# Kernel tuning notes

Measured on AMD Instinct MI355X. Metric: run time of the kernel, lower is better.

Reference implementation:

```python
import jax, jax.numpy as jnp
import numpy as np

# Module hyperparameters (from init_kwargs)
NUM_NEURONS = 16384
BATCH = 2048  # processed sequentially, sharing neuron state
V_TH0 = 1.0
V_RESET = 0.0
TAU = 20.0
DT = 1.0
ETA = 0.1
NOISE_STD = 0.1
MIN_TH = 0.5
MAX_TH = 2.0
USE_ADAPTIVE = True
STOCHASTIC = True


def setup_inputs() -> dict:
    key = jax.random.key(0)
    k1, k2 = jax.random.split(key)
    input_current = jax.random.normal(k1, (BATCH, NUM_NEURONS), dtype=jnp.float32)
    # stochastic membrane noise, pre-sampled for determinism
    noise = NOISE_STD * jax.random.normal(k2, (BATCH, NUM_NEURONS), dtype=jnp.float32)
    if not STOCHASTIC:
        noise = jnp.zeros_like(noise)
    return {"input_current": input_current, "noise": noise}


def reference(input_current, noise):
    # Faithful to the torch wrapper: each batch row is fed through the SAME
    # LIFNeuronGroup sequentially, carrying membrane potential V and the
    # adaptive threshold V_th across rows -> lax.scan over the batch axis.
    n = input_current.shape[1]
    V0 = jnp.full((n,), V_RESET, dtype=jnp.float32)
    Vth0 = jnp.full((n,), V_TH0, dtype=jnp.float32)

    def step(carry, inp):
        V, Vth = carry
        I, nz = inp
        # leaky integration + noise injection (fused elementwise)
        V = V + (DT / TAU) * (I - V) + nz
        spikes = V >= Vth
        V = jnp.where(spikes, V_RESET, V)
        if USE_ADAPTIVE:
            Vth = jnp.clip(Vth + ETA * spikes.astype(jnp.float32), MIN_TH, MAX_TH)
        return (V, Vth), spikes.astype(jnp.float32)

    (_, _), out_spikes = jax.lax.scan(step, (V0, Vth0), (input_current, noise))
    return out_spikes  # [batch, num_neurons] binary float32
```

## Files before the change

### kernel.cpp

```cpp
#include <hip/hip_runtime.h>


constexpr int N  = 16384;
constexpr int T  = 2048;
constexpr int U  = 16;
constexpr int NC = T / U;
constexpr int S  = 12;
constexpr int NP = 7;

__global__
__attribute__((amdgpu_flat_work_group_size(512, 512)))
void TorchLIFNeuronGroup_85152021610615_kernel(const float* __restrict__ I,
                                               const float* __restrict__ Z,
                                               float* __restrict__ O) {
    #pragma clang fp contract(off)
    __shared__ float ring[S][2][U][64];
    __shared__ int   flags[NC];
    __shared__ int   cons;

    if (threadIdx.x < NC) flags[threadIdx.x] = 0;
    if (threadIdx.x == 0) cons = -1;
    __syncthreads();

    const int wave = threadIdx.x >> 6;
    const int lane = threadIdx.x & 63;
    const int nb   = blockIdx.x * 64 + lane;

    if (wave >= 1) {
        const int p = wave - 1;
        const float* gI = I + nb;
        const float* gZ = Z + nb;

        for (int k = p; k < NC; k += NP) {
            while (__hip_atomic_load(&cons, __ATOMIC_RELAXED,
                                     __HIP_MEMORY_SCOPE_WORKGROUP) < k - S)
                __builtin_amdgcn_s_sleep(1);
            __asm__ volatile("" ::: "memory");

            const int    slot = k % S;
            const size_t t0   = (size_t)k * U;
            float vi[U], vz[U];
            #pragma unroll
            for (int u = 0; u < U; ++u) {
                vi[u] = gI[(t0 + u) * N];
                vz[u] = gZ[(t0 + u) * N];
            }
            #pragma unroll
            for (int u = 0; u < U; ++u) {
                ring[slot][0][u][lane] = vi[u];
                ring[slot][1][u][lane] = vz[u];
            }
            __asm__ volatile("s_waitcnt lgkmcnt(0)" ::: "memory");
            if (lane == 0)
                __hip_atomic_store(&flags[k], 1, __ATOMIC_RELAXED,
                                   __HIP_MEMORY_SCOPE_WORKGROUP);
        }

    } else {
        float* op = O + nb;
        float V   = 0.0f;
        float Vth = 1.0f;
        float ai[U], az[U], bi[U], bz[U];

        while (__hip_atomic_load(&flags[0], __ATOMIC_ACQUIRE,
                                 __HIP_MEMORY_SCOPE_WORKGROUP) == 0)
            __builtin_amdgcn_s_sleep(1);
        #pragma unroll
        for (int u = 0; u < U; ++u) { ai[u] = ring[0][0][u][lane]; az[u] = ring[0][1][u][lane]; }

        for (int k = 0; k < NC; k += 2) {
            while (__hip_atomic_load(&flags[k + 1], __ATOMIC_ACQUIRE,
                                     __HIP_MEMORY_SCOPE_WORKGROUP) == 0)
                __builtin_amdgcn_s_sleep(1);
            {
                const int slot = (k + 1) % S;
                #pragma unroll
                for (int u = 0; u < U; ++u) { bi[u] = ring[slot][0][u][lane]; bz[u] = ring[slot][1][u][lane]; }
            }
            #pragma unroll
            for (int u = 0; u < U; ++u) {
                #pragma clang fp contract(off)
                float d  = ai[u] - V;
                float v1 = V + 0.05f * d;
                float v2 = v1 + az[u];
                bool  s  = (v2 >= Vth);
                V = s ? 0.0f : v2;
                float nth = fminf(fmaxf(Vth + 0.1f, 0.5f), 2.0f);
                Vth = s ? nth : Vth;
                op[(size_t)(k * U + u) * N] = s ? 1.0f : 0.0f;
            }
            __asm__ volatile("s_waitcnt lgkmcnt(0)" ::: "memory");
            if (lane == 0)
                __hip_atomic_store(&cons, k, __ATOMIC_RELAXED,
                                   __HIP_MEMORY_SCOPE_WORKGROUP);

            if (k + 2 < NC) {
                while (__hip_atomic_load(&flags[k + 2], __ATOMIC_ACQUIRE,
                                         __HIP_MEMORY_SCOPE_WORKGROUP) == 0)
                    __builtin_amdgcn_s_sleep(1);
                const int slot = (k + 2) % S;
                #pragma unroll
                for (int u = 0; u < U; ++u) { ai[u] = ring[slot][0][u][lane]; az[u] = ring[slot][1][u][lane]; }
            }
            #pragma unroll
            for (int u = 0; u < U; ++u) {
                #pragma clang fp contract(off)
                float d  = bi[u] - V;
                float v1 = V + 0.05f * d;
                float v2 = v1 + bz[u];
                bool  s  = (v2 >= Vth);
                V = s ? 0.0f : v2;
                float nth = fminf(fmaxf(Vth + 0.1f, 0.5f), 2.0f);
                Vth = s ? nth : Vth;
                op[(size_t)((k + 1) * U + u) * N] = s ? 1.0f : 0.0f;
            }
            __asm__ volatile("s_waitcnt lgkmcnt(0)" ::: "memory");
            if (lane == 0)
                __hip_atomic_store(&cons, k + 1, __ATOMIC_RELAXED,
                                   __HIP_MEMORY_SCOPE_WORKGROUP);
        }
    }
}

extern "C" void kernel_launch(void* const* d_in, const int* in_sizes, int n_in,
                              void* d_out, int out_size, void* d_ws, size_t ws_size,
                              hipStream_t stream) {
    const float* input_current = (const float*)d_in[0];
    const float* noise         = (const float*)d_in[1];
    float* out                 = (float*)d_out;

    TorchLIFNeuronGroup_85152021610615_kernel<<<N / 64, 512, 0, stream>>>(
        input_current, noise, out);
}
```

Before: 326.4 us.

## Vectorize producer loads to float4, prefetch before ring wait, deepen ring

Producer waves now load input and noise as float4 tiles, with 16 lanes covering a 64-neuron row and four rows per wave. This replaces per-lane scalar loads, and the global loads are issued before the wait for a free ring slot so their latency overlaps the wait. The ring grows from 12 to 16 slots with power-of-two indexing. The consumer drops its mid-pair 'cons' publish and uses relaxed flag loads with compiler barriers. These changes are meant to cut load instruction count and stalls, in exchange for more LDS use and coarser slot-release granularity. Because loads now happen before the slot is confirmed free, correctness depends on the larger ring and the remaining per-pair cons update.

After: 343.9 us. 1.05x slower.

```diff
diff --git a/kernel.cpp b/kernel.cpp
--- a/kernel.cpp
+++ b/kernel.cpp
@@ -5,7 +5,7 @@
 constexpr int T  = 2048;
 constexpr int U  = 16;
 constexpr int NC = T / U;
-constexpr int S  = 12;
+constexpr int S  = 16;
 constexpr int NP = 7;
 
 __global__
@@ -14,7 +14,8 @@
                                                const float* __restrict__ Z,
                                                float* __restrict__ O) {
     #pragma clang fp contract(off)
-    __shared__ float ring[S][2][U][64];
+    __shared__ float ringI[S][U][64];
+    __shared__ float ringZ[S][U][64];
     __shared__ int   flags[NC];
     __shared__ int   cons;
 
@@ -24,31 +25,32 @@
 
     const int wave = threadIdx.x >> 6;
     const int lane = threadIdx.x & 63;
-    const int nb   = blockIdx.x * 64 + lane;
 
-    if (wave >= 1) {
+    if (wave != 0) {
         const int p = wave - 1;
-        const float* gI = I + nb;
-        const float* gZ = Z + nb;
+        const int r = lane >> 4;
+        const int c = lane & 15;
+        const float* bI = I + (size_t)blockIdx.x * 64 + 4 * c;
+        const float* bZ = Z + (size_t)blockIdx.x * 64 + 4 * c;
 
         for (int k = p; k < NC; k += NP) {
+            const int    slot = k & (S - 1);
+            const size_t row0 = (size_t)k * U + r;
+            float4 vi[4], vz[4];
+            #pragma unroll
+            for (int i = 0; i < 4; ++i) {
+                vi[i] = *(const float4*)(bI + (row0 + 4u * i) * N);
+                vz[i] = *(const float4*)(bZ + (row0 + 4u * i) * N);
+            }
+            __builtin_amdgcn_sched_barrier(0);
             while (__hip_atomic_load(&cons, __ATOMIC_RELAXED,
                                      __HIP_MEMORY_SCOPE_WORKGROUP) < k - S)
                 __builtin_amdgcn_s_sleep(1);
             __asm__ volatile("" ::: "memory");
-
-            const int    slot = k % S;
-            const size_t t0   = (size_t)k * U;
-            float vi[U], vz[U];
             #pragma unroll
-            for (int u = 0; u < U; ++u) {
-                vi[u] = gI[(t0 + u) * N];
-                vz[u] = gZ[(t0 + u) * N];
-            }
-            #pragma unroll
-            for (int u = 0; u < U; ++u) {
-                ring[slot][0][u][lane] = vi[u];
-                ring[slot][1][u][lane] = vz[u];
+            for (int i = 0; i < 4; ++i) {
+                *(float4*)&ringI[slot][4 * i + r][4 * c] = vi[i];
+                *(float4*)&ringZ[slot][4 * i + r][4 * c] = vz[i];
             }
             __asm__ volatile("s_waitcnt lgkmcnt(0)" ::: "memory");
             if (lane == 0)
@@ -57,25 +59,27 @@
         }
 
     } else {
-        float* op = O + nb;
+        float* op = O + (size_t)blockIdx.x * 64 + lane;
         float V   = 0.0f;
         float Vth = 1.0f;
         float ai[U], az[U], bi[U], bz[U];
 
-        while (__hip_atomic_load(&flags[0], __ATOMIC_ACQUIRE,
+        while (__hip_atomic_load(&flags[0], __ATOMIC_RELAXED,
                                  __HIP_MEMORY_SCOPE_WORKGROUP) == 0)
             __builtin_amdgcn_s_sleep(1);
+        __asm__ volatile("" ::: "memory");
         #pragma unroll
-        for (int u = 0; u < U; ++u) { ai[u] = ring[0][0][u][lane]; az[u] = ring[0][1][u][lane]; }
+        for (int u = 0; u < U; ++u) { ai[u] = ringI[0][u][lane]; az[u] = ringZ[0][u][lane]; }
 
         for (int k = 0; k < NC; k += 2) {
-            while (__hip_atomic_load(&flags[k + 1], __ATOMIC_ACQUIRE,
+            while (__hip_atomic_load(&flags[k + 1], __ATOMIC_RELAXED,
                                      __HIP_MEMORY_SCOPE_WORKGROUP) == 0)
                 __builtin_amdgcn_s_sleep(1);
+            __asm__ volatile("" ::: "memory");
             {
-                const int slot = (k + 1) % S;
+                const int slot = (k + 1) & (S - 1);
                 #pragma unroll
-                for (int u = 0; u < U; ++u) { bi[u] = ring[slot][0][u][lane]; bz[u] = ring[slot][1][u][lane]; }
+                for (int u = 0; u < U; ++u) { bi[u] = ringI[slot][u][lane]; bz[u] = ringZ[slot][u][lane]; }
             }
             #pragma unroll
             for (int u = 0; u < U; ++u) {
@@ -89,18 +93,14 @@
                 Vth = s ? nth : Vth;
                 op[(size_t)(k * U + u) * N] = s ? 1.0f : 0.0f;
             }
-            __asm__ volatile("s_waitcnt lgkmcnt(0)" ::: "memory");
-            if (lane == 0)
-                __hip_atomic_store(&cons, k, __ATOMIC_RELAXED,
-                                   __HIP_MEMORY_SCOPE_WORKGROUP);
-
             if (k + 2 < NC) {
-                while (__hip_atomic_load(&flags[k + 2], __ATOMIC_ACQUIRE,
+                while (__hip_atomic_load(&flags[k + 2], __ATOMIC_RELAXED,
                                          __HIP_MEMORY_SCOPE_WORKGROUP) == 0)
                     __builtin_amdgcn_s_sleep(1);
-                const int slot = (k + 2) % S;
+                __asm__ volatile("" ::: "memory");
+                const int slot = (k + 2) & (S - 1);
                 #pragma unroll
-                for (int u = 0; u < U; ++u) { ai[u] = ring[slot][0][u][lane]; az[u] = ring[slot][1][u][lane]; }
+                for (int u = 0; u < U; ++u) { ai[u] = ringI[slot][u][lane]; az[u] = ringZ[slot][u][lane]; }
             }
             #pragma unroll
             for (int u = 0; u < U; ++u) {
```
